# Optimization experiments

Hardware: AMD Instinct MI355X
Metric: run time of the kernel (lower is better)

The kernel has to match this reference:

```python
import jax, jax.numpy as jnp
import numpy as np

DIM = 96
HEADS = 3
WS = 7
N = WS * WS            # 49 tokens per window
C3 = 3 * DIM           # concatenated channel dim = 288
SCALE = (DIM // HEADS) ** -0.5  # torch uses dim//num_heads, NOT the effective head dim


def _relative_position_index():
    coords = np.stack(np.meshgrid(np.arange(WS), np.arange(WS), indexing='ij'))  # [2,WS,WS]
    flat = coords.reshape(2, -1)                     # [2,N]
    rel = flat[:, :, None] - flat[:, None, :]        # [2,N,N]
    rel = rel.transpose(1, 2, 0).astype(np.int64)    # [N,N,2]
    rel[:, :, 0] += WS - 1
    rel[:, :, 1] += WS - 1
    rel[:, :, 0] *= 2 * WS - 1
    return rel.sum(-1)                               # [N,N] int


def setup_inputs() -> dict:
    key = jax.random.key(0)
    ks = jax.random.split(key, 9)
    B = 4096
    nW = 64
    x = jax.random.normal(ks[0], (B, N, DIM), dtype=jnp.float32)
    y = jax.random.normal(ks[1], (B, N, DIM), dtype=jnp.float32)
    z = jax.random.normal(ks[2], (B, N, DIM), dtype=jnp.float32)
    mask = jax.random.normal(ks[3], (nW, N, N), dtype=jnp.float32)
    # Parameters (torch nn.Linear convention: out = in @ W.T + b)
    qkv_w = jax.random.normal(ks[4], (9 * DIM, C3), dtype=jnp.float32) * 0.02
    qkv_b = jnp.zeros((9 * DIM,), dtype=jnp.float32)
    proj_w = jax.random.normal(ks[5], (DIM, C3), dtype=jnp.float32) * 0.02
    proj_b = jnp.zeros((DIM,), dtype=jnp.float32)
    bias_table = jax.random.normal(ks[6], ((2 * WS - 1) * (2 * WS - 1), HEADS), dtype=jnp.float32) * 0.02
    rel_index = jnp.asarray(_relative_position_index(), dtype=jnp.int32)  # [N,N]
    return {"x": x, "y": y, "z": z, "mask": mask,
            "qkv_w": qkv_w, "qkv_b": qkv_b,
            "proj_w": proj_w, "proj_b": proj_b,
            "bias_table": bias_table, "rel_index": rel_index}


def reference(x, y, z, mask, qkv_w, qkv_b, proj_w, proj_b, bias_table, rel_index):
    B = x.shape[0]
    hd = C3 // HEADS  # effective per-head dim = 96
    xy = jnp.concatenate([x, y, z], axis=2)                 # [B,N,3C]
    qkv = xy @ qkv_w.T + qkv_b                              # [B,N,9C]
    qkv = qkv.reshape(B, N, 3, HEADS, hd).transpose(2, 0, 3, 1, 4)  # [3,B,H,N,hd]
    q, k, v = qkv[0], qkv[1], qkv[2]
    attn = jnp.einsum('bhnd,bhmd->bhnm', q * SCALE, k)      # [B,H,N,N]
    # relative position bias gather: [N*N,H] -> [H,N,N]
    bias = bias_table[rel_index.reshape(-1)].reshape(N, N, HEADS).transpose(2, 0, 1)
    attn = attn + bias[None]
    nW = mask.shape[0]
    attn = attn.reshape(B // nW, nW, HEADS, N, N) + mask[None, :, None]
    attn = attn.reshape(B, HEADS, N, N)
    attn = jax.nn.softmax(attn, axis=-1)
    out = jnp.einsum('bhnm,bhmd->bhnd', attn, v)            # [B,H,N,hd]
    out = out.transpose(0, 2, 1, 3).reshape(B, N, C3)       # [B,N,3C]
    out = out @ proj_w.T + proj_b                           # [B,N,C]
    return out
```

## Files before the change

### kernel.cpp

```cpp
#include <hip/hip_runtime.h>
#include <hip/hip_bf16.h>

#define NTOK 49

typedef __attribute__((ext_vector_type(8))) short short8;
typedef __attribute__((ext_vector_type(4))) float f32x4;

__device__ __forceinline__ unsigned short f2bf(float f) {
  union { float f; unsigned u; } v; v.f = f;
  unsigned r = v.u + 0x7FFFu + ((v.u >> 16) & 1u);
  return (unsigned short)(r >> 16);
}

__device__ __forceinline__ unsigned pk2bf(float a, float b) {
  __hip_bfloat162 h = __float22bfloat162_rn(float2{a, b});
  union { __hip_bfloat162 h; unsigned u; } c; c.h = h;
  return c.u;
}

__device__ __forceinline__ int vp_ix(int row, int col) {
  int gi = (col >> 3) ^ (row & 7);
  return row * 64 + (gi << 3) + (col & 7);
}

__global__ void prep_kernel(const float* __restrict__ qkv_w,
                            const float* __restrict__ bias_table,
                            const int* __restrict__ rel_index,
                            unsigned short* __restrict__ w_swz,
                            float* __restrict__ bias3)
{
  int idx = blockIdx.x * 256 + threadIdx.x;
  if (idx < 165888) {
    int f = idx >> 9, r = idx & 511;
    int l = r >> 3, j = r & 7;
    int nt = f / 9, ks = f - nt * 9;
    int row = nt * 16 + (l & 15);
    int k = ks * 32 + ((l >> 4) << 3) + j;
    w_swz[idx] = f2bf(qkv_w[row * 288 + k]);
  } else if (idx < 165888 + 7203) {
    int t = idx - 165888;
    int h = t / 2401, r = t - h * 2401;
    bias3[t] = bias_table[rel_index[r] * 3 + h];
  }
}

__global__ void prep2_kernel(const float* __restrict__ qkv_w,
                             const float* __restrict__ qkv_b,
                             const float* __restrict__ proj_w,
                             const float* __restrict__ proj_b,
                             unsigned short* __restrict__ w_swz,
                             float* __restrict__ cb)
{
  int idx = blockIdx.x * 256 + threadIdx.x;
  if (idx < 82944) {
    int f = idx >> 9, r = idx & 511;
    int l = r >> 3, j = r & 7;
    int hn = f / 9, ks = f - hn * 9;
    int h = hn / 6, ntd = hn - h * 6;
    int d = ntd * 16 + (l & 15);
    int k = ks * 32 + ((l >> 4) << 3) + j;
    const float* pr = proj_w + d * 288 + h * 96;
    const float* wr = qkv_w + (size_t)(576 + h * 96) * 288 + k;
    float s = 0.f;
    #pragma unroll 8
    for (int t = 0; t < 96; ++t) s += pr[t] * wr[(size_t)t * 288];
    w_swz[165888 + idx] = f2bf(s);
  } else if (idx < 82944 + 96) {
    int d = idx - 82944;
    float s = proj_b[d];
    #pragma unroll 1
    for (int h = 0; h < 3; ++h) {
      const float* pr = proj_w + d * 288 + h * 96;
      const float* bv = qkv_b + 576 + h * 96;
      #pragma unroll 8
      for (int t = 0; t < 96; ++t) s += pr[t] * bv[t];
    }
    cb[d] = s;
  }
}

#define A_OFF 0
#define Q_OFF 18432
#define K_OFF 23136
#define VT_OFF 27840
#define P_OFF 33984
#define SMEM_TOT 38080

__global__ __launch_bounds__(512, 4)
void wattn_kernel(const float* __restrict__ x, const float* __restrict__ y,
                  const float* __restrict__ z, const float* __restrict__ mask,
                  const float* __restrict__ qkv_b, const float* __restrict__ cb,
                  const unsigned short* __restrict__ w_swz,
                  const float* __restrict__ bias3,
                  float* __restrict__ out, int nW)
{
  __shared__ unsigned short smem[SMEM_TOT];
  const int b = blockIdx.x;
  const int tid = threadIdx.x;
  const int w = tid >> 6;
  const int lane = tid & 63;
  const int g = lane >> 4;
  const int cl = lane & 15;
  const int widx = b % nW;
  const int t4 = w & 3;
  const int hf = w >> 2;

  const int gx = ((g ^ ((cl >> 1) & 3)) << 3);
  const int c2 = (cl >> 2) & 1;
  const int gv = ((g ^ (cl & 3)) << 3);
  const int s0 = c2 << 5;
  const int s1 = 32 - s0;

  {
    const int row = tid >> 3;
    const int t7 = tid & 7;
    const int lb = row * 288 + (((t7 >> 1) ^ ((row >> 1) & 3)) << 3) + (t7 & 1) * 4;
    const size_t gb = ((size_t)b * NTOK + row) * 96 + t7 * 4;
    float4 v[9];
    if (row < NTOK) {
      #pragma unroll
      for (int k3 = 0; k3 < 3; ++k3) {
        v[0 + k3] = *(const float4*)(x + gb + k3 * 32);
        v[3 + k3] = *(const float4*)(y + gb + k3 * 32);
        v[6 + k3] = *(const float4*)(z + gb + k3 * 32);
      }
    } else {
      #pragma unroll
      for (int i = 0; i < 9; ++i) v[i] = make_float4(0.f, 0.f, 0.f, 0.f);
    }
    #pragma unroll
    for (int i = 0; i < 9; ++i) {
      uint2 d;
      d.x = pk2bf(v[i].x, v[i].y);
      d.y = pk2bf(v[i].z, v[i].w);
      *(uint2*)&smem[lb + (i / 3) * 96 + (i % 3) * 32] = d;
    }
  }

  const int tA = 2 * w;
  const int sA = (tA >= 12) ? 2 : ((tA >= 6) ? 1 : 0);
  const int dA = tA - 6 * sA, dB = dA + 1;
  const int mw = w & 3;
  const int d2t = 4 + (w >> 2);

  f32x4 outacc[3];
  #pragma unroll
  for (int i = 0; i < 3; ++i) outacc[i] = f32x4{0.f, 0.f, 0.f, 0.f};

  __syncthreads();

  #pragma unroll 1
  for (int h = 0; h < 3; ++h) {
    __syncthreads();

    {
      const unsigned short* abase = &smem[A_OFF + cl * 288 + gx];
      if (sA == 2) {
        #pragma unroll 1
        for (int t = 0; t < 2; ++t) {
          const int ntd = t ? dB : dA;
          const unsigned short* wp = w_swz + (size_t)(2 * 18 + h * 6 + ntd) * 9 * 512 + lane * 8;
          f32x4 acc[4];
          #pragma unroll
          for (int m = 0; m < 4; ++m) acc[m] = f32x4{0.f, 0.f, 0.f, 0.f};
          short8 bf = *(const short8*)(wp);
          #pragma unroll 1
          for (int ks = 0; ks < 8; ++ks) {
            short8 bfn = *(const short8*)(wp + (ks + 1) * 512);
            short8 af0 = *(const short8*)(abase + 0 * (16 * 288) + ks * 32);
            short8 af1 = *(const short8*)(abase + 1 * (16 * 288) + ks * 32);
            short8 af2 = *(const short8*)(abase + 2 * (16 * 288) + ks * 32);
            short8 af3 = *(const short8*)(abase + 3 * (16 * 288) + ks * 32);
            __builtin_amdgcn_s_setprio(1);
            acc[0] = __builtin_amdgcn_mfma_f32_16x16x32_bf16(af0, bf, acc[0], 0, 0, 0);
            acc[1] = __builtin_amdgcn_mfma_f32_16x16x32_bf16(af1, bf, acc[1], 0, 0, 0);
            acc[2] = __builtin_amdgcn_mfma_f32_16x16x32_bf16(af2, bf, acc[2], 0, 0, 0);
            acc[3] = __builtin_amdgcn_mfma_f32_16x16x32_bf16(af3, bf, acc[3], 0, 0, 0);
            __builtin_amdgcn_s_setprio(0);
            bf = bfn;
          }
          {
            short8 af0 = *(const short8*)(abase + 0 * (16 * 288) + 8 * 32);
            short8 af1 = *(const short8*)(abase + 1 * (16 * 288) + 8 * 32);
            short8 af2 = *(const short8*)(abase + 2 * (16 * 288) + 8 * 32);
            short8 af3 = *(const short8*)(abase + 3 * (16 * 288) + 8 * 32);
            __builtin_amdgcn_s_setprio(1);
            acc[0] = __builtin_amdgcn_mfma_f32_16x16x32_bf16(af0, bf, acc[0], 0, 0, 0);
            acc[1] = __builtin_amdgcn_mfma_f32_16x16x32_bf16(af1, bf, acc[1], 0, 0, 0);
            acc[2] = __builtin_amdgcn_mfma_f32_16x16x32_bf16(af2, bf, acc[2], 0, 0, 0);
            acc[3] = __builtin_amdgcn_mfma_f32_16x16x32_bf16(af3, bf, acc[3], 0, 0, 0);
            __builtin_amdgcn_s_setprio(0);
          }
          #pragma unroll
          for (int m = 0; m < 4; ++m) {
            uint2 d;
            d.x = pk2bf(acc[m][0], acc[m][1]);
            d.y = pk2bf(acc[m][2], acc[m][3]);
            *(uint2*)&smem[VT_OFF + vp_ix(ntd * 16 + cl, m * 16 + (g << 2))] = d;
          }
        }
      } else {
        const int s = sA;
        const int off = s ? K_OFF : Q_OFF;
        const float sc = s ? 1.f : 0.1767766952966369f;
        #pragma unroll 1
        for (int t = 0; t < 2; ++t) {
          const int ntd = t ? dB : dA;
          const unsigned short* wp = w_swz + (size_t)(s * 18 + h * 6 + ntd) * 9 * 512 + lane * 8;
          f32x4 acc[4];
          #pragma unroll
          for (int m = 0; m < 4; ++m) acc[m] = f32x4{0.f, 0.f, 0.f, 0.f};
          short8 bf = *(const short8*)(wp);
          #pragma unroll 1
          for (int ks = 0; ks < 8; ++ks) {
            short8 bfn = *(const short8*)(wp + (ks + 1) * 512);
            short8 af0 = *(const short8*)(abase + 0 * (16 * 288) + ks * 32);
            short8 af1 = *(const short8*)(abase + 1 * (16 * 288) + ks * 32);
            short8 af2 = *(const short8*)(abase + 2 * (16 * 288) + ks * 32);
            short8 af3 = *(const short8*)(abase + 3 * (16 * 288) + ks * 32);
            __builtin_amdgcn_s_setprio(1);
            acc[0] = __builtin_amdgcn_mfma_f32_16x16x32_bf16(bf, af0, acc[0], 0, 0, 0);
            acc[1] = __builtin_amdgcn_mfma_f32_16x16x32_bf16(bf, af1, acc[1], 0, 0, 0);
            acc[2] = __builtin_amdgcn_mfma_f32_16x16x32_bf16(bf, af2, acc[2], 0, 0, 0);
            acc[3] = __builtin_amdgcn_mfma_f32_16x16x32_bf16(bf, af3, acc[3], 0, 0, 0);
            __builtin_amdgcn_s_setprio(0);
            bf = bfn;
          }
          {
            short8 af0 = *(const short8*)(abase + 0 * (16 * 288) + 8 * 32);
            short8 af1 = *(const short8*)(abase + 1 * (16 * 288) + 8 * 32);
            short8 af2 = *(const short8*)(abase + 2 * (16 * 288) + 8 * 32);
            short8 af3 = *(const short8*)(abase + 3 * (16 * 288) + 8 * 32);
            __builtin_amdgcn_s_setprio(1);
            acc[0] = __builtin_amdgcn_mfma_f32_16x16x32_bf16(bf, af0, acc[0], 0, 0, 0);
            acc[1] = __builtin_amdgcn_mfma_f32_16x16x32_bf16(bf, af1, acc[1], 0, 0, 0);
            acc[2] = __builtin_amdgcn_mfma_f32_16x16x32_bf16(bf, af2, acc[2], 0, 0, 0);
            acc[3] = __builtin_amdgcn_mfma_f32_16x16x32_bf16(bf, af3, acc[3], 0, 0, 0);
            __builtin_amdgcn_s_setprio(0);
          }
          const int d0 = ntd * 16 + (g << 2);
          float4 bq4 = *(const float4*)&qkv_b[s * 288 + h * 96 + d0];
          #pragma unroll
          for (int m = 0; m < 4; ++m) {
            int token = m * 16 + cl;
            uint2 dd;
            dd.x = pk2bf((acc[m][0] + bq4.x) * sc, (acc[m][1] + bq4.y) * sc);
            dd.y = pk2bf((acc[m][2] + bq4.z) * sc, (acc[m][3] + bq4.w) * sc);
            if (token < NTOK) {
              int gi = (d0 >> 3) ^ ((token >> 1) & 3);
              *(uint2*)&smem[off + token * 96 + (gi << 3) + (d0 & 7)] = dd;
            }
          }
        }
      }
    }

    {
      f32x4 acc2 = f32x4{0, 0, 0, 0};
      const unsigned short* wpC = w_swz + (size_t)(36 + h * 6 + d2t) * 9 * 512 + lane * 8;
      const unsigned short* abase2 = &smem[A_OFF + (mw * 16 + cl) * 288 + gx];
      short8 bf = *(const short8*)(wpC);
      #pragma unroll 1
      for (int ks = 0; ks < 8; ++ks) {
        short8 bfn = *(const short8*)(wpC + (ks + 1) * 512);
        short8 af = *(const short8*)(abase2 + ks * 32);
        acc2 = __builtin_amdgcn_mfma_f32_16x16x32_bf16(af, bf, acc2, 0, 0, 0);
        bf = bfn;
      }
      {
        short8 af = *(const short8*)(abase2 + 8 * 32);
        acc2 = __builtin_amdgcn_mfma_f32_16x16x32_bf16(af, bf, acc2, 0, 0, 0);
      }
      uint2 d;
      d.x = pk2bf(acc2[0], acc2[1]);
      d.y = pk2bf(acc2[2], acc2[3]);
      *(uint2*)&smem[VT_OFF + vp_ix(d2t * 16 + cl, mw * 16 + (g << 2))] = d;
    }
    __syncthreads();

    float bi[2][4], mk[2][4];
    #pragma unroll
    for (int rr = 0; rr < 2; ++rr) {
      int n = t4 * 16 + (g << 2) + 2 * hf + rr;
      int nn = n < NTOK ? n : NTOK - 1;
      const float* brow = bias3 + h * 2401 + nn * 49;
      const float* mrow = mask + ((size_t)widx * NTOK + nn) * NTOK;
      #pragma unroll
      for (int nt = 0; nt < 4; ++nt) {
        int mm = nt * 16 + cl;
        mm = mm < NTOK ? mm : NTOK - 1;
        bi[rr][nt] = brow[mm];
        mk[rr][nt] = mrow[mm];
      }
    }

    f32x4 sacc[4];
    #pragma unroll
    for (int nt = 0; nt < 4; ++nt) sacc[nt] = f32x4{0.f, 0.f, 0.f, 0.f};
    {
      const unsigned short* qbase = &smem[Q_OFF + (t4 * 16 + cl) * 96 + gx];
      const unsigned short* kbase = &smem[K_OFF + cl * 96 + gx];
      #pragma unroll 1
      for (int ks = 0; ks < 3; ++ks) {
        short8 aq = *(const short8*)(qbase + ks * 32);
        short8 bk0 = *(const short8*)(kbase + 0 * (16 * 96) + ks * 32);
        short8 bk1 = *(const short8*)(kbase + 1 * (16 * 96) + ks * 32);
        short8 bk2 = *(const short8*)(kbase + 2 * (16 * 96) + ks * 32);
        short8 bk3 = *(const short8*)(kbase + 3 * (16 * 96) + ks * 32);
        __builtin_amdgcn_s_setprio(1);
        sacc[0] = __builtin_amdgcn_mfma_f32_16x16x32_bf16(aq, bk0, sacc[0], 0, 0, 0);
        sacc[1] = __builtin_amdgcn_mfma_f32_16x16x32_bf16(aq, bk1, sacc[1], 0, 0, 0);
        sacc[2] = __builtin_amdgcn_mfma_f32_16x16x32_bf16(aq, bk2, sacc[2], 0, 0, 0);
        sacc[3] = __builtin_amdgcn_mfma_f32_16x16x32_bf16(aq, bk3, sacc[3], 0, 0, 0);
        __builtin_amdgcn_s_setprio(0);
      }
    }

    #pragma unroll
    for (int r = 0; r < 4; ++r) {
      if ((r >> 1) != hf) continue;
      const int rr = r & 1;
      int n = t4 * 16 + (g << 2) + r;
      float vals[4];
      float mx = -1e30f;
      #pragma unroll
      for (int nt = 0; nt < 4; ++nt) {
        int m = nt * 16 + cl;
        float sv = -1e30f;
        if (m < NTOK) sv = sacc[nt][r] + bi[rr][nt] + mk[rr][nt];
        vals[nt] = sv;
        mx = fmaxf(mx, sv);
      }
      mx = fmaxf(mx, __shfl_xor(mx, 1));
      mx = fmaxf(mx, __shfl_xor(mx, 2));
      mx = fmaxf(mx, __shfl_xor(mx, 4));
      mx = fmaxf(mx, __shfl_xor(mx, 8));
      float sum = 0.f;
      #pragma unroll
      for (int nt = 0; nt < 4; ++nt) {
        float e = __expf(vals[nt] - mx);
        vals[nt] = e;
        sum += e;
      }
      sum += __shfl_xor(sum, 1);
      sum += __shfl_xor(sum, 2);
      sum += __shfl_xor(sum, 4);
      sum += __shfl_xor(sum, 8);
      float inv = 1.f / sum;
      unsigned d01 = pk2bf(vals[0] * inv, vals[1] * inv);
      unsigned d23 = pk2bf(vals[2] * inv, vals[3] * inv);
      smem[P_OFF + vp_ix(n, 0 * 16 + cl)] = (unsigned short)d01;
      smem[P_OFF + vp_ix(n, 1 * 16 + cl)] = (unsigned short)(d01 >> 16);
      smem[P_OFF + vp_ix(n, 2 * 16 + cl)] = (unsigned short)d23;
      smem[P_OFF + vp_ix(n, 3 * 16 + cl)] = (unsigned short)(d23 >> 16);
    }
    __syncthreads();

    {
      const unsigned short* pbase = &smem[P_OFF + (t4 * 16 + cl) * 64 + gv];
      const unsigned short* vbase = &smem[VT_OFF + (hf * 3 * 16 + cl) * 64 + gv];
      #pragma unroll
      for (int ks = 0; ks < 2; ++ks) {
        const int ko = ks ? s1 : s0;
        short8 ap = *(const short8*)(pbase + ko);
        short8 bv0 = *(const short8*)(vbase + 0 * (16 * 64) + ko);
        short8 bv1 = *(const short8*)(vbase + 1 * (16 * 64) + ko);
        short8 bv2 = *(const short8*)(vbase + 2 * (16 * 64) + ko);
        __builtin_amdgcn_s_setprio(1);
        outacc[0] = __builtin_amdgcn_mfma_f32_16x16x32_bf16(bv0, ap, outacc[0], 0, 0, 0);
        outacc[1] = __builtin_amdgcn_mfma_f32_16x16x32_bf16(bv1, ap, outacc[1], 0, 0, 0);
        outacc[2] = __builtin_amdgcn_mfma_f32_16x16x32_bf16(bv2, ap, outacc[2], 0, 0, 0);
        __builtin_amdgcn_s_setprio(0);
      }
    }
  }

  {
    int n = t4 * 16 + cl;
    if (n < NTOK) {
      size_t ob = ((size_t)b * NTOK + n) * 96;
      #pragma unroll
      for (int jj = 0; jj < 3; ++jj) {
        int d0 = (hf * 3 + jj) * 16 + (g << 2);
        float4 c4 = *(const float4*)&cb[d0];
        float4 o;
        o.x = outacc[jj][0] + c4.x;
        o.y = outacc[jj][1] + c4.y;
        o.z = outacc[jj][2] + c4.z;
        o.w = outacc[jj][3] + c4.w;
        *(float4*)&out[ob + d0] = o;
      }
    }
  }
}

extern "C" void kernel_launch(void* const* d_in, const int* in_sizes, int n_in,
                              void* d_out, int out_size, void* d_ws, size_t ws_size,
                              hipStream_t stream) {
  const float* x          = (const float*)d_in[0];
  const float* y          = (const float*)d_in[1];
  const float* z          = (const float*)d_in[2];
  const float* mask       = (const float*)d_in[3];
  const float* qkv_w      = (const float*)d_in[4];
  const float* qkv_b      = (const float*)d_in[5];
  const float* proj_w     = (const float*)d_in[6];
  const float* proj_b     = (const float*)d_in[7];
  const float* bias_table = (const float*)d_in[8];
  const int*   rel_index  = (const int*)d_in[9];

  int B  = in_sizes[0] / (NTOK * 96);
  int nW = in_sizes[3] / (NTOK * NTOK);

  unsigned short* w_swz = (unsigned short*)d_ws;
  float*          bias3 = (float*)(w_swz + 248832);
  float*          cbv   = bias3 + 7203;

  prep_kernel<<<677, 256, 0, stream>>>(qkv_w, bias_table, rel_index, w_swz, bias3);
  prep2_kernel<<<325, 256, 0, stream>>>(qkv_w, qkv_b, proj_w, proj_b, w_swz, cbv);
  wattn_kernel<<<B, 512, 0, stream>>>(x, y, z, mask, qkv_b, cbv,
                                      w_swz, bias3, (float*)d_out, nW);
}
```

Measured before the change: 287.8 us.

## Fuse bias+mask into a precomputed table and drop the post-softmax barrier

The prep kernel now builds a per-head, per-window table holding relative position bias plus mask, so the attention kernel does one load per score instead of two. Softmax is now computed for all four rows by both waves sharing a row stripe, so each wave owns every P row it later reads. That lets the `__syncthreads` between the P write and the PV MFMA be removed. The cost is twice the softmax work, a benign race where both waves write identical P values, and a larger workspace table built on each call.

```diff
diff --git a/kernel.cpp b/kernel.cpp
--- a/kernel.cpp
+++ b/kernel.cpp
@@ -26,8 +26,9 @@
 __global__ void prep_kernel(const float* __restrict__ qkv_w,
                             const float* __restrict__ bias_table,
                             const int* __restrict__ rel_index,
+                            const float* __restrict__ mask,
                             unsigned short* __restrict__ w_swz,
-                            float* __restrict__ bias3)
+                            float* __restrict__ bm3, int nW)
 {
   int idx = blockIdx.x * 256 + threadIdx.x;
   if (idx < 165888) {
@@ -37,10 +38,16 @@
     int row = nt * 16 + (l & 15);
     int k = ks * 32 + ((l >> 4) << 3) + j;
     w_swz[idx] = f2bf(qkv_w[row * 288 + k]);
-  } else if (idx < 165888 + 7203) {
+  } else {
     int t = idx - 165888;
-    int h = t / 2401, r = t - h * 2401;
-    bias3[t] = bias_table[rel_index[r] * 3 + h];
+    if (t < 3 * 64 * 2401) {
+      int h = t / (64 * 2401);
+      int r = t - h * (64 * 2401);
+      int wi = r / 2401;
+      int nm = r - wi * 2401;
+      float bv = bias_table[rel_index[nm] * 3 + h];
+      bm3[t] = bv + mask[(size_t)wi * 2401 + nm];
+    }
   }
 }
 
@@ -88,10 +95,10 @@
 
 __global__ __launch_bounds__(512, 4)
 void wattn_kernel(const float* __restrict__ x, const float* __restrict__ y,
-                  const float* __restrict__ z, const float* __restrict__ mask,
+                  const float* __restrict__ z,
                   const float* __restrict__ qkv_b, const float* __restrict__ cb,
                   const unsigned short* __restrict__ w_swz,
-                  const float* __restrict__ bias3,
+                  const float* __restrict__ bm3,
                   float* __restrict__ out, int nW)
 {
   __shared__ unsigned short smem[SMEM_TOT];
@@ -278,19 +285,20 @@
     }
     __syncthreads();
 
-    float bi[2][4], mk[2][4];
-    #pragma unroll
-    for (int rr = 0; rr < 2; ++rr) {
-      int n = t4 * 16 + (g << 2) + 2 * hf + rr;
-      int nn = n < NTOK ? n : NTOK - 1;
-      const float* brow = bias3 + h * 2401 + nn * 49;
-      const float* mrow = mask + ((size_t)widx * NTOK + nn) * NTOK;
-      #pragma unroll
-      for (int nt = 0; nt < 4; ++nt) {
-        int mm = nt * 16 + cl;
-        mm = mm < NTOK ? mm : NTOK - 1;
-        bi[rr][nt] = brow[mm];
-        mk[rr][nt] = mrow[mm];
+    float bm[4][4];
+    {
+      const float* bmb = bm3 + ((size_t)(h * nW + widx)) * 2401;
+      #pragma unroll
+      for (int rr = 0; rr < 4; ++rr) {
+        int n = t4 * 16 + (g << 2) + rr;
+        int nn = n < NTOK ? n : NTOK - 1;
+        const float* brow = bmb + nn * 49;
+        #pragma unroll
+        for (int nt = 0; nt < 4; ++nt) {
+          int mm = nt * 16 + cl;
+          mm = mm < NTOK ? mm : NTOK - 1;
+          bm[rr][nt] = brow[mm];
+        }
       }
     }
 
@@ -318,8 +326,6 @@
 
     #pragma unroll
     for (int r = 0; r < 4; ++r) {
-      if ((r >> 1) != hf) continue;
-      const int rr = r & 1;
       int n = t4 * 16 + (g << 2) + r;
       float vals[4];
       float mx = -1e30f;
@@ -327,7 +333,7 @@
       for (int nt = 0; nt < 4; ++nt) {
         int m = nt * 16 + cl;
         float sv = -1e30f;
-        if (m < NTOK) sv = sacc[nt][r] + bi[rr][nt] + mk[rr][nt];
+        if (m < NTOK) sv = sacc[nt][r] + bm[r][nt];
         vals[nt] = sv;
         mx = fmaxf(mx, sv);
       }
@@ -354,7 +360,6 @@
       smem[P_OFF + vp_ix(n, 2 * 16 + cl)] = (unsigned short)d23;
       smem[P_OFF + vp_ix(n, 3 * 16 + cl)] = (unsigned short)(d23 >> 16);
     }
-    __syncthreads();
 
     {
       const unsigned short* pbase = &smem[P_OFF + (t4 * 16 + cl) * 64 + gv];
@@ -412,11 +417,13 @@
   int nW = in_sizes[3] / (NTOK * NTOK);
 
   unsigned short* w_swz = (unsigned short*)d_ws;
-  float*          bias3 = (float*)(w_swz + 248832);
-  float*          cbv   = bias3 + 7203;
-
-  prep_kernel<<<677, 256, 0, stream>>>(qkv_w, bias_table, rel_index, w_swz, bias3);
+  float*          bm3   = (float*)(w_swz + 248832);
+  float*          cbv   = bm3 + (size_t)3 * nW * 2401;
+
+  int prep1_elems = 165888 + 3 * nW * 2401;
+  prep_kernel<<<(prep1_elems + 255) / 256, 256, 0, stream>>>(
+      qkv_w, bias_table, rel_index, mask, w_swz, bm3, nW);
   prep2_kernel<<<325, 256, 0, stream>>>(qkv_w, qkv_b, proj_w, proj_b, w_swz, cbv);
-  wattn_kernel<<<B, 512, 0, stream>>>(x, y, z, mask, qkv_b, cbv,
-                                      w_swz, bias3, (float*)d_out, nW);
-}
+  wattn_kernel<<<B, 512, 0, stream>>>(x, y, z, qkv_b, cbv,
+                                      w_swz, bm3, (float*)d_out, nW);
+}
```

New measurement: 298.9 us. 1.04x slower.
